# Optimization experiments

Measured on AMD Instinct MI355X. Metric: run time of the kernel, lower is better.

Reference implementation:

```python
import jax, jax.numpy as jnp
import numpy as np

N, B, S, BW, IC = 512, 4, 31, 11, 32

def gelu(x):
    return jax.nn.gelu(x, approximate=False)

def conv2d(x, w, b, pad, groups=1):
    y = jax.lax.conv_general_dilated(x, w, (1, 1), [(pad, pad), (pad, pad)],
        dimension_numbers=('NCHW', 'OIHW', 'NCHW'), feature_group_count=groups)
    return y + b[None, :, None, None]

def extract_windows(fmap, pos, win):
    C, H, W = fmap.shape[1:]
    r = win // 2
    cx = jnp.round(pos[:, 0]).astype(jnp.int32)
    cy = jnp.round(pos[:, 1]).astype(jnp.int32)
    off = jnp.arange(win, dtype=jnp.int32) - r
    ys = jnp.clip(cy[:, None] + off[None, :], 0, H - 1)
    xs = jnp.clip(cx[:, None] + off[None, :], 0, W - 1)
    w = fmap[0][:, ys[:, :, None], xs[:, None, :]]
    return jnp.transpose(w, (1, 0, 2, 3))

def _forward(bottleneck, vis_stem, spv, ppb,
             ic1_w, ic1_b, ic2_w, ic2_b, ic3_w, ic3_b,
             cnx_dw_w, cnx_dw_b, cnx_ln_w, cnx_ln_b,
             cnx_pw1_w, cnx_pw1_b, cnx_pw2_w, cnx_pw2_b, cnx_gamma,
             bnp_w, bnp_b, band_embed, film_w, film_b,
             dec1_w, dec1_b, dec2_w, dec2_b, dec3_w, dec3_b,
             tile_h, tile_w, fused_h, fused_w, vis_h, vis_w):
    n = spv.shape[0]
    # intrinsic path: per-source stem window -> 3 convs
    sw = extract_windows(vis_stem, spv, S)                 # [N,64,S,S]
    h = gelu(conv2d(sw, ic1_w, ic1_b, 1))
    h = gelu(conv2d(h, ic2_w, ic2_b, 1))
    intrinsic = conv2d(h, ic3_w, ic3_b, 1)                 # [N,IC,S,S]
    # bottleneck context path (vis px -> fused px: scale by vis_scale/fused_scale)
    scale = 0.1 / 0.4
    pbn = spv * scale
    pbn = jnp.stack([jnp.clip(pbn[:, 0], 0.0, fused_w - 1.0),
                     jnp.clip(pbn[:, 1], 0.0, fused_h - 1.0)], axis=-1)
    bwin = extract_windows(bottleneck, pbn, BW)            # [N,256,BW,BW]
    d = conv2d(bwin, cnx_dw_w, cnx_dw_b, 3, groups=bwin.shape[1])
    d = jnp.transpose(d, (0, 2, 3, 1))                     # NHWC
    mu = d.mean(-1, keepdims=True)
    var = ((d - mu) ** 2).mean(-1, keepdims=True)
    d = (d - mu) / jnp.sqrt(var + 1e-6) * cnx_ln_w + cnx_ln_b
    d = gelu(d @ cnx_pw1_w.T + cnx_pw1_b)
    d = (d @ cnx_pw2_w.T + cnx_pw2_b) * cnx_gamma
    bwin = bwin + jnp.transpose(d, (0, 3, 1, 2))
    bn_feat = gelu(conv2d(bwin, bnp_w, bnp_b, 0))          # [N,64,BW,BW]
    # fixed gaussian-weighted pooling (sigma=0.4 on [-1,1] grid)
    lin = jnp.linspace(-1.0, 1.0, BW)
    yy, xx = jnp.meshgrid(lin, lin, indexing='ij')
    g = jnp.exp(-(xx ** 2 + yy ** 2) / (2 * 0.4 ** 2))
    g = g / g.sum()
    bn_vec = (bn_feat * g[None, None]).sum((-2, -1))       # [N,64]
    # FiLM conditioning
    tile_pos = jnp.clip(jnp.stack([ppb[..., 0] / max(tile_w - 1.0, 1.0),
                                   ppb[..., 1] / max(tile_h - 1.0, 1.0)], -1), 0.0, 1.0)
    sub_px = ppb - jnp.round(ppb)
    band_e = jnp.broadcast_to(band_embed[None], (n, B, band_embed.shape[1]))
    bn_nb = jnp.broadcast_to(bn_vec[:, None], (n, B, bn_vec.shape[1]))
    cond = jnp.concatenate([band_e, tile_pos, sub_px, bn_nb], axis=-1)  # [N,B,84]
    film = cond @ film_w.T + film_b                        # [N,B,2*IC]
    gamma = 1.0 + film[..., :IC]
    beta = film[..., IC:]
    mod = intrinsic[:, None] * gamma[..., None, None] + beta[..., None, None]
    mod = gelu(mod).reshape(n * B, IC, S, S)
    o = gelu(conv2d(mod, dec1_w, dec1_b, 1))
    o = gelu(conv2d(o, dec2_w, dec2_b, 1))
    o = conv2d(o, dec3_w, dec3_b, 0).reshape(n, B, S, S)
    o = jax.nn.softplus(o)
    sums = jnp.maximum(o.sum((-2, -1), keepdims=True), 1e-8)
    return o / sums

def setup_inputs():
    key = jax.random.key(0)
    ks = jax.random.split(key, 24)
    FH = FW = 256; VH = VW = 1024; TH = TW = 1024
    f32 = jnp.float32
    nrm = lambda k, shp, s=0.05: jax.random.normal(k, shp, dtype=f32) * s
    return {
        'bottleneck': nrm(ks[0], (1, 256, FH, FW), 1.0),
        'vis_stem': nrm(ks[1], (1, 64, VH, VW), 1.0),
        'source_positions_vis': jax.random.uniform(ks[2], (N, 2), dtype=f32, minval=0.0, maxval=VW - 1.0),
        'positions_per_band': jax.random.uniform(ks[3], (N, B, 2), dtype=f32, minval=0.0, maxval=TW - 1.0),
        'ic1_w': nrm(ks[4], (64, 64, 3, 3)), 'ic1_b': jnp.zeros((64,), f32),
        'ic2_w': nrm(ks[5], (64, 64, 3, 3)), 'ic2_b': jnp.zeros((64,), f32),
        'ic3_w': nrm(ks[6], (IC, 64, 3, 3)), 'ic3_b': jnp.zeros((IC,), f32),
        'cnx_dw_w': nrm(ks[7], (256, 1, 7, 7)), 'cnx_dw_b': jnp.zeros((256,), f32),
        'cnx_ln_w': jnp.ones((256,), f32), 'cnx_ln_b': jnp.zeros((256,), f32),
        'cnx_pw1_w': nrm(ks[8], (1024, 256)), 'cnx_pw1_b': jnp.zeros((1024,), f32),
        'cnx_pw2_w': nrm(ks[9], (256, 1024)), 'cnx_pw2_b': jnp.zeros((256,), f32),
        'cnx_gamma': jnp.full((256,), 0.1, f32),
        'bnp_w': nrm(ks[10], (64, 256, 1, 1)), 'bnp_b': jnp.zeros((64,), f32),
        'band_embed': nrm(ks[11], (B, 16), 1.0),
        'film_w': nrm(ks[12], (2 * IC, 84)), 'film_b': jnp.zeros((2 * IC,), f32),
        'dec1_w': nrm(ks[13], (32, IC, 3, 3)), 'dec1_b': jnp.zeros((32,), f32),
        'dec2_w': nrm(ks[14], (32, 32, 3, 3)), 'dec2_b': jnp.zeros((32,), f32),
        'dec3_w': nrm(ks[15], (1, 32, 1, 1)), 'dec3_b': jnp.zeros((1,), f32),
        'tile_h': TH, 'tile_w': TW, 'fused_h': FH, 'fused_w': FW, 'vis_h': VH, 'vis_w': VW,
    }

def reference(bottleneck, vis_stem, source_positions_vis, positions_per_band, ic1_w, ic1_b, ic2_w, ic2_b, ic3_w, ic3_b, cnx_dw_w, cnx_dw_b, cnx_ln_w, cnx_ln_b, cnx_pw1_w, cnx_pw1_b, cnx_pw2_w, cnx_pw2_b, cnx_gamma, bnp_w, bnp_b, band_embed, film_w, film_b, dec1_w, dec1_b, dec2_w, dec2_b, dec3_w, dec3_b, tile_h, tile_w, fused_h, fused_w, vis_h, vis_w):
    return _forward(bottleneck, vis_stem, source_positions_vis, positions_per_band, ic1_w, ic1_b, ic2_w, ic2_b, ic3_w, ic3_b, cnx_dw_w, cnx_dw_b, cnx_ln_w, cnx_ln_b, cnx_pw1_w, cnx_pw1_b, cnx_pw2_w, cnx_pw2_b, cnx_gamma, bnp_w, bnp_b, band_embed, film_w, film_b, dec1_w, dec1_b, dec2_w, dec2_b, dec3_w, dec3_b, tile_h, tile_w, fused_h, fused_w, vis_h, vis_w)
```

## Files before the change

### kernel.cpp

```cpp
#include <hip/hip_runtime.h>
#include <cstdint>
#include <cstddef>
#include <cmath>

#define DEV __device__ __forceinline__

typedef __attribute__((ext_vector_type(8))) short bf16x8;
typedef __attribute__((ext_vector_type(4))) float f32x4;

DEV float erf_fast(float x){
  float ax = fabsf(x);
  float t = __builtin_amdgcn_rcpf(fmaf(0.3275911f, ax, 1.f));
  float p = t*fmaf(t, fmaf(t, fmaf(t, fmaf(t, 1.061405429f, -1.453152027f),
             1.421413741f), -0.284496736f), 0.254829592f);
  float e = __expf(-ax*ax);
  float r = fmaf(-p, e, 1.f);
  return x >= 0.f ? r : -r;
}
DEV float gelu_f(float x){ return 0.5f*x*(1.0f + erf_fast(x*0.7071067811865476f)); }
DEV float softplus_f(float x){ return fmaxf(x,0.f) + log1pf(expf(-fabsf(x))); }
DEV unsigned short f2bf(float x){
  unsigned u = __float_as_uint(x);
  unsigned r = (u + 0x7fffu + ((u>>16)&1u)) >> 16;
  return (unsigned short)r;
}
DEV float bf2f(unsigned short h){
  unsigned u = ((unsigned)h) << 16;
  return __uint_as_float(u);
}

struct PackJobs {
  const float* src[8];
  unsigned short* dst[8];
  int ntn[8], ntk[8], K[8], conv[8], base[8];
};

__global__ __launch_bounds__(256) void packall_k(PackJobs J)
{
  int blk = blockIdx.x;
  int j = 0;
#pragma unroll
  for (int i=1;i<8;++i) if (blk >= J.base[i]) j = i;
  int tid = (blk - J.base[j])*256 + threadIdx.x;
  const int ntk = J.ntk[j], K = J.K[j];
  int total = J.ntn[j]*ntk*64;
  if (tid >= total) return;
  int lane = tid & 63;
  int f = tid >> 6;
  int kt = f % ntk, nt = f / ntk;
  int row = nt*16 + (lane & 15);
  int k0 = kt*32 + (lane >> 4)*8;
  const float* src = J.src[j];
  unsigned short h[8];
  if (J.conv[j]) {
    const int Cin = K;
#pragma unroll
    for (int q=0;q<8;++q) {
      int k = k0 + q;
      int s = k / Cin;
      int ic = k - s*Cin;
      h[q] = f2bf(src[((size_t)row*Cin + ic)*9 + s]);
    }
  } else {
#pragma unroll
    for (int q=0;q<8;++q) h[q] = f2bf(src[(size_t)row*K + k0 + q]);
  }
  uint4 pk;
  pk.x = (unsigned)h[0] | ((unsigned)h[1]<<16);
  pk.y = (unsigned)h[2] | ((unsigned)h[3]<<16);
  pk.z = (unsigned)h[4] | ((unsigned)h[5]<<16);
  pk.w = (unsigned)h[6] | ((unsigned)h[7]<<16);
  *reinterpret_cast<uint4*>(J.dst[j] + (size_t)tid*8) = pk;
}

__global__ __launch_bounds__(256) void dwt_k(const float* __restrict__ w,
                                             float* __restrict__ wT)
{
  int k = blockIdx.x;
  int ch = threadIdx.x;
  wT[k*256 + ch] = w[(size_t)ch*49 + k];
}

__global__ __launch_bounds__(256) void extvwin_k(const float* __restrict__ vis,
                                                 const float* __restrict__ spv,
                                                 unsigned short* __restrict__ vwin)
{
  int il = blockIdx.x;
  int p = blockIdx.y*256 + threadIdx.x;
  if (p >= 1089) return;
  int wy = p/33, wx = p%33;
  unsigned short* dst = vwin + ((size_t)il*1089 + p)*64;
  if (wy==0 || wy==32 || wx==0 || wx==32) {
    uint4 z = {0,0,0,0};
#pragma unroll
    for (int q=0;q<8;++q) *reinterpret_cast<uint4*>(dst + q*8) = z;
    return;
  }
  int cx = (int)rintf(spv[il*2+0]);
  int cy = (int)rintf(spv[il*2+1]);
  int gy = min(max(cy + wy - 16, 0), 1023);
  int gx = min(max(cx + wx - 16, 0), 1023);
  const float* sp = vis + (size_t)gy*1024 + gx;
  unsigned short h[64];
#pragma unroll
  for (int c=0;c<64;++c) h[c] = f2bf(sp[(size_t)c<<20]);
#pragma unroll
  for (int q=0;q<8;++q) {
    uint4 pk;
    pk.x = (unsigned)h[q*8+0] | ((unsigned)h[q*8+1]<<16);
    pk.y = (unsigned)h[q*8+2] | ((unsigned)h[q*8+3]<<16);
    pk.z = (unsigned)h[q*8+4] | ((unsigned)h[q*8+5]<<16);
    pk.w = (unsigned)h[q*8+6] | ((unsigned)h[q*8+7]<<16);
    *reinterpret_cast<uint4*>(dst + q*8) = pk;
  }
}

template<int CIN, int COUT, int NKT, int MODE, bool FGELU>
__global__ __launch_bounds__(256,3) void convmf_k(
    const unsigned short* __restrict__ src,
    const unsigned short* __restrict__ Wp,
    const float* __restrict__ Bv,
    unsigned short* __restrict__ out)
{
  constexpr int NOCT = COUT/16;
  constexpr int NSLOT = CIN/8;
  constexpr int SWM = NSLOT-1;
  const int item = blockIdx.x;
  const int y0 = blockIdx.y*8;
  const int t = threadIdx.x;
  const int w = t>>6, l = t&63, g = l>>4, l15 = l&15;

  __shared__ __align__(16) unsigned short lds[330*CIN];

  for (int u = t; u < 330*NSLOT; u += 256) {
    int slot = u & SWM;
    int rowi = u / NSLOT;
    int r = rowi / 33, col = rowi - r*33;
    uint4 val = {0,0,0,0};
    if (MODE==1) {
      int gr = y0 + r;
      if (gr < 33)
        val = *reinterpret_cast<const uint4*>(src + ((size_t)item*1089 + gr*33 + col)*CIN + slot*8);
    } else {
      int y = y0 + r - 1, x = col - 1;
      if ((unsigned)y < 31u && (unsigned)x < 31u)
        val = *reinterpret_cast<const uint4*>(src + ((size_t)item*961 + y*31 + x)*CIN + slot*8);
    }
    int ds = slot ^ (rowi & SWM);
    *reinterpret_cast<uint4*>(&lds[rowi*CIN + ds*8]) = val;
  }
  __syncthreads();

  int pbase[4], gpos[4]; bool pvalid[4];
#pragma unroll
  for (int pt=0; pt<4; ++pt) {
    int p = (w*4+pt)*16 + l15;
    int pc = min(p, 247);
    int py = pc/31, px = pc - py*31;
    pbase[pt] = py*33 + px;
    gpos[pt] = y0*31 + p;
    pvalid[pt] = (p < 248) && (gpos[pt] < 961);
  }

  f32x4 acc[NOCT][4];
#pragma unroll
  for (int o=0;o<NOCT;++o)
#pragma unroll
    for (int pt=0;pt<4;++pt) acc[o][pt] = (f32x4){0.f,0.f,0.f,0.f};

  bf16x8 wcur[NOCT];
#pragma unroll
  for (int o=0;o<NOCT;++o)
    wcur[o] = *reinterpret_cast<const bf16x8*>(Wp + ((size_t)(o*NKT)*64 + l)*8);

  for (int kt=0; kt<NKT; ++kt) {
    bf16x8 wnxt[NOCT];
    if (kt+1 < NKT) {
#pragma unroll
      for (int o=0;o<NOCT;++o)
        wnxt[o] = *reinterpret_cast<const bf16x8*>(Wp + ((size_t)(o*NKT+kt+1)*64 + l)*8);
    }
    int k0 = kt*32 + g*8;
    int s = k0 / CIN;
    int icg = (k0 - s*CIN) >> 3;
    int roff = (s/3)*33 + (s - (s/3)*3);
    bf16x8 bf[4];
#pragma unroll
    for (int pt=0; pt<4; ++pt) {
      int rowi = pbase[pt] + roff;
      int ds = icg ^ (rowi & SWM);
      bf[pt] = *reinterpret_cast<const bf16x8*>(&lds[rowi*CIN + ds*8]);
    }
#pragma unroll
    for (int o=0; o<NOCT; ++o) {
#pragma unroll
      for (int pt=0; pt<4; ++pt)
        acc[o][pt] = __builtin_amdgcn_mfma_f32_16x16x32_bf16(wcur[o], bf[pt], acc[o][pt], 0,0,0);
    }
    if (kt+1 < NKT) {
#pragma unroll
      for (int o=0;o<NOCT;++o) wcur[o] = wnxt[o];
    }
  }

#pragma unroll
  for (int o=0; o<NOCT; ++o) {
    float4 bv4 = *reinterpret_cast<const float4*>(Bv + o*16 + g*4);
#pragma unroll
    for (int pt=0; pt<4; ++pt) {
      if (!pvalid[pt]) continue;
      float v0 = acc[o][pt][0] + bv4.x;
      float v1 = acc[o][pt][1] + bv4.y;
      float v2 = acc[o][pt][2] + bv4.z;
      float v3 = acc[o][pt][3] + bv4.w;
      if (FGELU) { v0=gelu_f(v0); v1=gelu_f(v1); v2=gelu_f(v2); v3=gelu_f(v3); }
      uint2 pk;
      pk.x = (unsigned)f2bf(v0) | ((unsigned)f2bf(v1)<<16);
      pk.y = (unsigned)f2bf(v2) | ((unsigned)f2bf(v3)<<16);
      *reinterpret_cast<uint2*>(out + ((size_t)item*961 + gpos[pt])*COUT + o*16 + g*4) = pk;
    }
  }
}

__global__ __launch_bounds__(256,3) void decfused_k(
    const unsigned short* __restrict__ intc,
    const unsigned short* __restrict__ Wp1, const float* __restrict__ B1,
    const unsigned short* __restrict__ Wp2, const float* __restrict__ B2,
    const float* __restrict__ film,
    const float* __restrict__ w3, const float* __restrict__ b3,
    float* __restrict__ outf, float* __restrict__ sums)
{
  const int item = blockIdx.x;
  const int y0 = blockIdx.y*8;
  const int t = threadIdx.x;
  const int w = t>>6, l = t&63, g = l>>4, l15 = l&15;

  __shared__ __align__(16) unsigned short ldsA[12*33*32];
  __shared__ __align__(16) unsigned short ldsB[10*33*32];

  const int sit = item >> 2;
  const float* frow = film + (size_t)item*64;

  for (int u=t; u<1320; u+=256)
    *reinterpret_cast<uint4*>(ldsB + u*8) = (uint4){0,0,0,0};

  for (int u=t; u<1584; u+=256) {
    int slot = u & 3;
    int rowi = u >> 2;
    int r = rowi/33, col = rowi - r*33;
    int y = y0 + r - 2, x = col - 1;
    uint4 val = {0,0,0,0};
    if ((unsigned)y < 31u && (unsigned)x < 31u) {
      val = *reinterpret_cast<const uint4*>(intc + ((size_t)sit*961 + y*31 + x)*32 + slot*8);
      int c0 = slot*8;
      float4 g0 = *reinterpret_cast<const float4*>(frow + c0);
      float4 g1 = *reinterpret_cast<const float4*>(frow + c0 + 4);
      float4 b0 = *reinterpret_cast<const float4*>(frow + 32 + c0);
      float4 b1 = *reinterpret_cast<const float4*>(frow + 32 + c0 + 4);
      unsigned short x8[8] = {
        (unsigned short)(val.x&0xffff),(unsigned short)(val.x>>16),
        (unsigned short)(val.y&0xffff),(unsigned short)(val.y>>16),
        (unsigned short)(val.z&0xffff),(unsigned short)(val.z>>16),
        (unsigned short)(val.w&0xffff),(unsigned short)(val.w>>16)};
      unsigned short o8[8];
      o8[0]=f2bf(gelu_f(fmaf(bf2f(x8[0]), 1.f+g0.x, b0.x)));
      o8[1]=f2bf(gelu_f(fmaf(bf2f(x8[1]), 1.f+g0.y, b0.y)));
      o8[2]=f2bf(gelu_f(fmaf(bf2f(x8[2]), 1.f+g0.z, b0.z)));
      o8[3]=f2bf(gelu_f(fmaf(bf2f(x8[3]), 1.f+g0.w, b0.w)));
      o8[4]=f2bf(gelu_f(fmaf(bf2f(x8[4]), 1.f+g1.x, b1.x)));
      o8[5]=f2bf(gelu_f(fmaf(bf2f(x8[5]), 1.f+g1.y, b1.y)));
      o8[6]=f2bf(gelu_f(fmaf(bf2f(x8[6]), 1.f+g1.z, b1.z)));
      o8[7]=f2bf(gelu_f(fmaf(bf2f(x8[7]), 1.f+g1.w, b1.w)));
      val.x = (unsigned)o8[0] | ((unsigned)o8[1]<<16);
      val.y = (unsigned)o8[2] | ((unsigned)o8[3]<<16);
      val.z = (unsigned)o8[4] | ((unsigned)o8[5]<<16);
      val.w = (unsigned)o8[6] | ((unsigned)o8[7]<<16);
    }
    int ds = slot ^ (rowi & 3);
    *reinterpret_cast<uint4*>(&ldsA[rowi*32 + ds*8]) = val;
  }
  __syncthreads();

  {
    int pbase[5], rowB[5]; bool pv[5];
#pragma unroll
    for (int pt=0; pt<5; ++pt) {
      int pd = (w*5+pt)*16 + l15;
      int pc = min(pd, 309);
      int ry = pc/31, rx = pc - ry*31;
      pbase[pt] = ry*33 + rx;
      rowB[pt] = ry*33 + rx + 1;
      int gy = y0 - 1 + ry;
      pv[pt] = (pd < 310) && ((unsigned)gy < 31u);
    }
    f32x4 a1[2][5];
#pragma unroll
    for (int o=0;o<2;++o)
#pragma unroll
      for (int pt=0;pt<5;++pt) a1[o][pt] = (f32x4){0.f,0.f,0.f,0.f};

    for (int kt=0; kt<9; ++kt) {
      int roff = (kt/3)*33 + (kt - (kt/3)*3);
      bf16x8 bf[5];
#pragma unroll
      for (int pt=0; pt<5; ++pt) {
        int rowi = pbase[pt] + roff;
        int ds = g ^ (rowi & 3);
        bf[pt] = *reinterpret_cast<const bf16x8*>(&ldsA[rowi*32 + ds*8]);
      }
#pragma unroll
      for (int o=0; o<2; ++o) {
        bf16x8 af = *reinterpret_cast<const bf16x8*>(Wp1 + ((size_t)(o*9+kt)*64 + l)*8);
#pragma unroll
        for (int pt=0; pt<5; ++pt)
          a1[o][pt] = __builtin_amdgcn_mfma_f32_16x16x32_bf16(af, bf[pt], a1[o][pt], 0,0,0);
      }
    }
#pragma unroll
    for (int o=0; o<2; ++o) {
      float4 bv4 = *reinterpret_cast<const float4*>(B1 + o*16 + g*4);
      int sl = o*2 + (g>>1);
#pragma unroll
      for (int pt=0; pt<5; ++pt) {
        if (!pv[pt]) continue;
        float v0 = gelu_f(a1[o][pt][0] + bv4.x);
        float v1 = gelu_f(a1[o][pt][1] + bv4.y);
        float v2 = gelu_f(a1[o][pt][2] + bv4.z);
        float v3 = gelu_f(a1[o][pt][3] + bv4.w);
        uint2 pk;
        pk.x = (unsigned)f2bf(v0) | ((unsigned)f2bf(v1)<<16);
        pk.y = (unsigned)f2bf(v2) | ((unsigned)f2bf(v3)<<16);
        int phys = sl ^ (rowB[pt] & 3);
        *reinterpret_cast<uint2*>(&ldsB[rowB[pt]*32 + phys*8 + (g&1)*4]) = pk;
      }
    }
  }
  __syncthreads();

  float bsum = 0.f;
  {
    int pbase[4], gpos[4]; bool pv[4];
#pragma unroll
    for (int pt=0; pt<4; ++pt) {
      int pd = (w*4+pt)*16 + l15;
      int pc = min(pd, 247);
      int py = pc/31, px = pc - py*31;
      pbase[pt] = py*33 + px;
      gpos[pt] = y0*31 + pd;
      pv[pt] = (pd < 248) && (gpos[pt] < 961);
    }
    f32x4 a2[2][4];
#pragma unroll
    for (int o=0;o<2;++o)
#pragma unroll
      for (int pt=0;pt<4;++pt) a2[o][pt] = (f32x4){0.f,0.f,0.f,0.f};

    for (int kt=0; kt<9; ++kt) {
      int roff = (kt/3)*33 + (kt - (kt/3)*3);
      bf16x8 bf[4];
#pragma unroll
      for (int pt=0; pt<4; ++pt) {
        int rowi = pbase[pt] + roff;
        int ds = g ^ (rowi & 3);
        bf[pt] = *reinterpret_cast<const bf16x8*>(&ldsB[rowi*32 + ds*8]);
      }
#pragma unroll
      for (int o=0; o<2; ++o) {
        bf16x8 af = *reinterpret_cast<const bf16x8*>(Wp2 + ((size_t)(o*9+kt)*64 + l)*8);
#pragma unroll
        for (int pt=0; pt<4; ++pt)
          a2[o][pt] = __builtin_amdgcn_mfma_f32_16x16x32_bf16(af, bf[pt], a2[o][pt], 0,0,0);
      }
    }

    float w3r[8];
#pragma unroll
    for (int o=0;o<2;++o) {
      float4 wv = *reinterpret_cast<const float4*>(w3 + o*16 + g*4);
      w3r[o*4+0]=wv.x; w3r[o*4+1]=wv.y; w3r[o*4+2]=wv.z; w3r[o*4+3]=wv.w;
    }
    float b3v = b3[0];
#pragma unroll
    for (int pt=0; pt<4; ++pt) {
      float part = 0.f;
#pragma unroll
      for (int o=0; o<2; ++o) {
        float4 bv4 = *reinterpret_cast<const float4*>(B2 + o*16 + g*4);
        float v0 = gelu_f(a2[o][pt][0] + bv4.x);
        float v1 = gelu_f(a2[o][pt][1] + bv4.y);
        float v2 = gelu_f(a2[o][pt][2] + bv4.z);
        float v3 = gelu_f(a2[o][pt][3] + bv4.w);
        part += v0*w3r[o*4+0] + v1*w3r[o*4+1] + v2*w3r[o*4+2] + v3*w3r[o*4+3];
      }
      part += __shfl_xor(part, 16);
      part += __shfl_xor(part, 32);
      float sp = softplus_f(part + b3v);
      if (pv[pt] && g==0) {
        outf[(size_t)item*961 + gpos[pt]] = sp;
        bsum += sp;
      }
    }
  }
  {
    float* redf = reinterpret_cast<float*>(ldsA);
    redf[t] = bsum;
    __syncthreads();
    for (int off=128; off>0; off>>=1) {
      if (t < off) redf[t] += redf[t+off];
      __syncthreads();
    }
    if (t==0) atomicAdd(&sums[item], redf[0]);
  }
}

__global__ __launch_bounds__(256,4) void dwfused4_k(
    const float* __restrict__ bott, const float* __restrict__ spv,
    const float* __restrict__ wT, const float* __restrict__ b,
    unsigned short* __restrict__ bwinT, unsigned short* __restrict__ dwout)
{
  const int n = blockIdx.x, cs = blockIdx.y*64, t = threadIdx.x;
  __shared__ float tile[121*66];

  float pxf = fminf(fmaxf(spv[n*2+0]*0.25f, 0.f), 255.f);
  float pyf = fminf(fmaxf(spv[n*2+1]*0.25f, 0.f), 255.f);
  int cx = (int)rintf(pxf), cy = (int)rintf(pyf);

  for (int idx=t; idx<121*32; idx+=256) {
    int j = idx/121, p = idx - j*121;
    int y = p/11, x = p - y*11;
    int gy = min(max(cy + y - 5, 0), 255);
    int gx = min(max(cx + x - 5, 0), 255);
    const float* s0 = bott + ((size_t)(cs+2*j)<<16) + (gy<<8) + gx;
    *reinterpret_cast<float2*>(&tile[p*66 + 2*j]) = (float2){s0[0], s0[65536]};
  }
  __syncthreads();

  for (int idx=t; idx<121*64; idx+=256) {
    int p = idx >> 6, c = idx & 63;
    bwinT[((size_t)n*121 + p)*256 + cs + c] = f2bf(tile[p*66 + c]);
  }

  const int c = t & 63, ph = t >> 6;
  const int ch = cs + c;
  const float bias = b[ch];

  for (int y=ph; y<11; y+=4) {
    float acc[11];
#pragma unroll
    for (int x=0;x<11;++x) acc[x] = bias;
#pragma unroll
    for (int dy=0; dy<7; ++dy) {
      int yy = y + dy - 3;
      if ((unsigned)yy < 11u) {
        float r[11];
#pragma unroll
        for (int k=0;k<11;++k) r[k] = tile[(yy*11+k)*66 + c];
        float w7[7];
#pragma unroll
        for (int j=0;j<7;++j) w7[j] = wT[(dy*7+j)*256 + ch];
#pragma unroll
        for (int x=0;x<11;++x) {
#pragma unroll
          for (int dx=0;dx<7;++dx) {
            int xx = x + dx - 3;
            if (xx >= 0 && xx < 11)
              acc[x] = fmaf(r[xx], w7[dx], acc[x]);
          }
        }
      }
    }
#pragma unroll
    for (int x=0;x<11;++x)
      dwout[((size_t)n*121 + y*11 + x)*256 + ch] = f2bf(acc[x]);
  }
}

__global__ __launch_bounds__(512,4) void cnx_mfma3_k(
    const unsigned short* __restrict__ xin,
    const float* __restrict__ lnw, const float* __restrict__ lnb,
    const unsigned short* __restrict__ W1p, const float* __restrict__ B1,
    const unsigned short* __restrict__ W2p, const float* __restrict__ B2,
    const float* __restrict__ gvec,
    const unsigned short* __restrict__ bwinT,
    const unsigned short* __restrict__ Wbp, const float* __restrict__ bnpb,
    float* __restrict__ bnv, float inv_gsum)
{
  const int t = threadIdx.x;
  const int w = t >> 6;
  const int l = t & 63;
  const int g = l >> 4;
  const int l15 = l & 15;
  const int row0 = blockIdx.x * 64;

  __shared__ __align__(16) unsigned short xs[64*264];
  __shared__ __align__(16) unsigned short hs[64*136];

  {
    const int rl = t >> 3, q = t & 7;
    const unsigned short* xr = xin + (size_t)(row0+rl)*256 + q*32;
    float xv[32]; float s = 0.f, s2 = 0.f;
#pragma unroll
    for (int i=0;i<32;i+=8){
      uint4 v = *reinterpret_cast<const uint4*>(xr+i);
      unsigned short xh[8] = {
        (unsigned short)(v.x&0xffff),(unsigned short)(v.x>>16),
        (unsigned short)(v.y&0xffff),(unsigned short)(v.y>>16),
        (unsigned short)(v.z&0xffff),(unsigned short)(v.z>>16),
        (unsigned short)(v.w&0xffff),(unsigned short)(v.w>>16)};
#pragma unroll
      for (int j=0;j<8;++j){
        float f = bf2f(xh[j]);
        xv[i+j] = f; s += f; s2 += f*f;
      }
    }
    s += __shfl_xor(s,1); s2 += __shfl_xor(s2,1);
    s += __shfl_xor(s,2); s2 += __shfl_xor(s2,2);
    s += __shfl_xor(s,4); s2 += __shfl_xor(s2,4);
    float mu = s*(1.f/256.f);
    float rstd = rsqrtf(s2*(1.f/256.f) - mu*mu + 1e-6f);
#pragma unroll
    for (int i=0;i<32;i+=8){
      int c = q*32 + i;
      float4 w0 = *reinterpret_cast<const float4*>(lnw+c);
      float4 w1 = *reinterpret_cast<const float4*>(lnw+c+4);
      float4 b0 = *reinterpret_cast<const float4*>(lnb+c);
      float4 b1 = *reinterpret_cast<const float4*>(lnb+c+4);
      unsigned short h[8];
      h[0]=f2bf(fmaf((xv[i+0]-mu)*rstd, w0.x, b0.x));
      h[1]=f2bf(fmaf((xv[i+1]-mu)*rstd, w0.y, b0.y));
      h[2]=f2bf(fmaf((xv[i+2]-mu)*rstd, w0.z, b0.z));
      h[3]=f2bf(fmaf((xv[i+3]-mu)*rstd, w0.w, b0.w));
      h[4]=f2bf(fmaf((xv[i+4]-mu)*rstd, w1.x, b1.x));
      h[5]=f2bf(fmaf((xv[i+5]-mu)*rstd, w1.y, b1.y));
      h[6]=f2bf(fmaf((xv[i+6]-mu)*rstd, w1.z, b1.z));
      h[7]=f2bf(fmaf((xv[i+7]-mu)*rstd, w1.w, b1.w));
      uint4 pk;
      pk.x = (unsigned)h[0] | ((unsigned)h[1]<<16);
      pk.y = (unsigned)h[2] | ((unsigned)h[3]<<16);
      pk.z = (unsigned)h[4] | ((unsigned)h[5]<<16);
      pk.w = (unsigned)h[6] | ((unsigned)h[7]<<16);
      *reinterpret_cast<uint4*>(&xs[rl*264 + c]) = pk;
    }
  }
  __syncthreads();

  f32x4 acc2[8];
#pragma unroll
  for (int i=0;i<8;++i) acc2[i] = (f32x4){0.f,0.f,0.f,0.f};

  for (int hc=0; hc<8; ++hc) {
    const int ht = hc*8 + w;
    f32x4 acc1[4];
#pragma unroll
    for (int i=0;i<4;++i) acc1[i] = (f32x4){0.f,0.f,0.f,0.f};

#pragma unroll
    for (int kt=0; kt<8; ++kt) {
      bf16x8 xf[4];
#pragma unroll
      for (int rt=0; rt<4; ++rt)
        xf[rt] = *reinterpret_cast<const bf16x8*>(&xs[(rt*16+l15)*264 + kt*32 + g*8]);
      bf16x8 wf = *reinterpret_cast<const bf16x8*>(W1p + ((size_t)(ht*8+kt)*64 + l)*8);
#pragma unroll
      for (int rt=0; rt<4; ++rt)
        acc1[rt] = __builtin_amdgcn_mfma_f32_16x16x32_bf16(wf, xf[rt], acc1[rt], 0,0,0);
    }
    {
      const int hb = hc*128 + w*16 + 4*g;
      float4 b1v = *reinterpret_cast<const float4*>(B1 + hb);
#pragma unroll
      for (int rt=0; rt<4; ++rt) {
        unsigned short h0 = f2bf(gelu_f(acc1[rt][0] + b1v.x));
        unsigned short h1 = f2bf(gelu_f(acc1[rt][1] + b1v.y));
        unsigned short h2 = f2bf(gelu_f(acc1[rt][2] + b1v.z));
        unsigned short h3 = f2bf(gelu_f(acc1[rt][3] + b1v.w));
        uint2 pk;
        pk.x = (unsigned)h0 | ((unsigned)h1<<16);
        pk.y = (unsigned)h2 | ((unsigned)h3<<16);
        *reinterpret_cast<uint2*>(&hs[(rt*16+l15)*136 + w*16 + 4*g]) = pk;
      }
    }
    __syncthreads();
#pragma unroll
    for (int kt=0; kt<4; ++kt) {
      bf16x8 hf[4];
#pragma unroll
      for (int rt=0; rt<4; ++rt)
        hf[rt] = *reinterpret_cast<const bf16x8*>(&hs[(rt*16+l15)*136 + kt*32 + g*8]);
#pragma unroll
      for (int cj=0; cj<2; ++cj) {
        const int ct = 2*w + cj;
        bf16x8 wf = *reinterpret_cast<const bf16x8*>(W2p + ((size_t)(ct*32 + hc*4 + kt)*64 + l)*8);
#pragma unroll
        for (int rt=0; rt<4; ++rt)
          acc2[cj*4+rt] = __builtin_amdgcn_mfma_f32_16x16x32_bf16(hf[rt], wf, acc2[cj*4+rt], 0,0,0);
      }
    }
    __syncthreads();
  }

#pragma unroll
  for (int cj=0; cj<2; ++cj) {
    const int c = (2*w+cj)*16 + l15;
    const float b2 = B2[c], gm = gvec[c];
#pragma unroll
    for (int rt=0; rt<4; ++rt) {
#pragma unroll
      for (int reg=0; reg<4; ++reg) {
        int row = rt*16 + 4*g + reg;
        float res = bf2f(bwinT[(size_t)(row0+row)*256 + c]) + (acc2[cj*4+rt][reg] + b2)*gm;
        xs[row*264 + c] = f2bf(res);
      }
    }
  }
  __syncthreads();

  {
    const int oct = w & 3;
    f32x4 abn[2];
#pragma unroll
    for (int i=0;i<2;++i) abn[i] = (f32x4){0.f,0.f,0.f,0.f};
#pragma unroll
    for (int kt=0; kt<8; ++kt) {
      bf16x8 bfw = *reinterpret_cast<const bf16x8*>(Wbp + ((size_t)(oct*8+kt)*64 + l)*8);
#pragma unroll
      for (int i=0;i<2;++i) {
        const int rt = (w>>2) + 2*i;
        bf16x8 af = *reinterpret_cast<const bf16x8*>(&xs[(rt*16+l15)*264 + kt*32 + g*8]);
        abn[i] = __builtin_amdgcn_mfma_f32_16x16x32_bf16(af, bfw, abn[i], 0,0,0);
      }
    }

    float* red = reinterpret_cast<float*>(hs);
#pragma unroll
    for (int i=0;i<2;++i) {
      const int rt = (w>>2) + 2*i;
      float bv = bnpb[oct*16 + l15];
#pragma unroll
      for (int reg=0; reg<4; ++reg) {
        int lr = rt*16 + g*4 + reg;
        int p = (row0 + lr) % 121;
        int py=p/11, px=p-py*11;
        float ly=-1.f+0.2f*py, lx=-1.f+0.2f*px;
        float wg = __expf(-(lx*lx+ly*ly)/0.32f) * inv_gsum;
        red[lr*64 + oct*16 + l15] = gelu_f(abn[i][reg] + bv) * wg;
      }
    }
  }
  __syncthreads();
  {
    float* red = reinterpret_cast<float*>(hs);
    int oc = t & 63, seg = t >> 6;
    float s = 0.f;
    int curn = (row0 + seg*8) / 121;
    for (int i=0;i<8;++i) {
      int row = seg*8 + i;
      int n = (row0 + row) / 121;
      if (n != curn) { atomicAdd(&bnv[curn*64 + oc], s); s = 0.f; curn = n; }
      s += red[row*64 + oc];
    }
    atomicAdd(&bnv[curn*64 + oc], s);
  }
}

__global__ __launch_bounds__(256) void film_k(
    const float* __restrict__ bn_vec, const float* __restrict__ ppb,
    const float* __restrict__ bemb, const float* __restrict__ fw,
    const float* __restrict__ fb, float* __restrict__ film)
{
  int n = blockIdx.x, t = threadIdx.x;
  __shared__ float cond[4][84];
  for (int i=t; i<4*84; i+=256) {
    int b = i/84, j = i%84;
    float v;
    if (j < 16) v = bemb[b*16 + j];
    else if (j == 16) { float p = ppb[((size_t)n*4+b)*2+0]; v = fminf(fmaxf(p*(1.f/1023.f),0.f),1.f); }
    else if (j == 17) { float p = ppb[((size_t)n*4+b)*2+1]; v = fminf(fmaxf(p*(1.f/1023.f),0.f),1.f); }
    else if (j == 18) { float p = ppb[((size_t)n*4+b)*2+0]; v = p - rintf(p); }
    else if (j == 19) { float p = ppb[((size_t)n*4+b)*2+1]; v = p - rintf(p); }
    else v = bn_vec[n*64 + (j-20)];
    cond[b][j] = v;
  }
  __syncthreads();
  int b = t >> 6, oc = t & 63;
  float s = fb[oc];
  for (int j=0;j<84;++j) s = fmaf(cond[b][j], fw[oc*84+j], s);
  film[((size_t)n*4+b)*64 + oc] = s;
}

__global__ __launch_bounds__(256) void norm_k(float* __restrict__ out,
                                              const float* __restrict__ sums)
{
  int il = blockIdx.x;
  int p = blockIdx.y*256 + threadIdx.x;
  if (p < 961) {
    float inv = 1.f / fmaxf(sums[il], 1e-8f);
    out[(size_t)il*961 + p] *= inv;
  }
}

extern "C" void kernel_launch(void* const* d_in, const int* in_sizes, int n_in,
                              void* d_out, int out_size, void* d_ws, size_t ws_size,
                              hipStream_t stream)
{
  const float* bott = (const float*)d_in[0];
  const float* vis  = (const float*)d_in[1];
  const float* spv  = (const float*)d_in[2];
  const float* ppb  = (const float*)d_in[3];
  const float* ic1w = (const float*)d_in[4];  const float* ic1b = (const float*)d_in[5];
  const float* ic2w = (const float*)d_in[6];  const float* ic2b = (const float*)d_in[7];
  const float* ic3w = (const float*)d_in[8];  const float* ic3b = (const float*)d_in[9];
  const float* dww  = (const float*)d_in[10]; const float* dwb  = (const float*)d_in[11];
  const float* lnw  = (const float*)d_in[12]; const float* lnb  = (const float*)d_in[13];
  const float* pw1w = (const float*)d_in[14]; const float* pw1b = (const float*)d_in[15];
  const float* pw2w = (const float*)d_in[16]; const float* pw2b = (const float*)d_in[17];
  const float* cgam = (const float*)d_in[18];
  const float* bnpw = (const float*)d_in[19]; const float* bnpb = (const float*)d_in[20];
  const float* bemb = (const float*)d_in[21];
  const float* fw   = (const float*)d_in[22]; const float* fb   = (const float*)d_in[23];
  const float* d1w  = (const float*)d_in[24]; const float* d1b  = (const float*)d_in[25];
  const float* d2w  = (const float*)d_in[26]; const float* d2b  = (const float*)d_in[27];
  const float* d3w  = (const float*)d_in[28]; const float* d3b  = (const float*)d_in[29];
  float* out = (float*)d_out;

  char* ws = (char*)d_ws;

  const int CH = (ws_size >= 116500000ull) ? 256 : 128;

  unsigned short* bwinT = (unsigned short*)(ws);
  unsigned short* dwout = (unsigned short*)(ws + 31719424);
  unsigned short* vwin = (unsigned short*)(ws);
  size_t o_bufA = (size_t)CH*139392;
  size_t o_bufB = o_bufA + (size_t)CH*123008;
  size_t o_bufI = o_bufB + (size_t)CH*123008;
  size_t p1end  = o_bufI + (size_t)CH*61504;
  unsigned short* bufA = (unsigned short*)(ws + o_bufA);
  unsigned short* bufB = (unsigned short*)(ws + o_bufB);
  unsigned short* bufI = (unsigned short*)(ws + o_bufI);
  size_t tail = (p1end > 63438848ull) ? p1end : 63438848ull;

  float* bnv  = (float*)(ws + tail);
  float* sums = (float*)(ws + tail + 131072);
  float* film = (float*)(ws + tail + 139264);
  unsigned short* W1p = (unsigned short*)(ws + tail + 663552);
  unsigned short* W2p = (unsigned short*)(ws + tail + 1187840);
  unsigned short* Wbp = (unsigned short*)(ws + tail + 1712128);
  unsigned short* Pc1 = (unsigned short*)(ws + tail + 1744896);
  unsigned short* Pc2 = (unsigned short*)(ws + tail + 1818624);
  unsigned short* Pc3 = (unsigned short*)(ws + tail + 1892352);
  unsigned short* Pd1 = (unsigned short*)(ws + tail + 1929216);
  unsigned short* Pd2 = (unsigned short*)(ws + tail + 1947648);
  float* dwwT = (float*)(ws + tail + 1966080);

  {
    PackJobs J;
    const float* srcs[8] = {pw1w, pw2w, bnpw, ic1w, ic2w, ic3w, d1w, d2w};
    unsigned short* dsts[8] = {W1p, W2p, Wbp, Pc1, Pc2, Pc3, Pd1, Pd2};
    int ntns[8] = {64,16,4, 4,4,2, 2,2};
    int ntks[8] = {8,32,8, 18,18,18, 9,9};
    int Ks[8]   = {256,1024,256, 64,64,64, 32,32};
    int convs[8]= {0,0,0, 1,1,1, 1,1};
    int base = 0;
    for (int i=0;i<8;++i) {
      J.src[i]=srcs[i]; J.dst[i]=dsts[i]; J.ntn[i]=ntns[i]; J.ntk[i]=ntks[i];
      J.K[i]=Ks[i]; J.conv[i]=convs[i]; J.base[i]=base;
      base += (ntns[i]*ntks[i]*64 + 255)/256;
    }
    packall_k<<<base,256,0,stream>>>(J);
  }
  dwt_k<<<49,256,0,stream>>>(dww, dwwT);

  hipMemsetAsync(ws + tail, 0, 139264, stream);

  float gs = 0.f;
  for (int py=0; py<11; ++py) for (int px=0; px<11; ++px) {
    float ly=-1.f+0.2f*py, lx=-1.f+0.2f*px;
    gs += expf(-(lx*lx+ly*ly)/0.32f);
  }
  const float inv_gsum = 1.f/gs;

  dwfused4_k<<<dim3(512,4),256,0,stream>>>(bott, spv, dwwT, dwb, bwinT, dwout);
  cnx_mfma3_k<<<968,512,0,stream>>>(dwout, lnw,lnb, W1p,pw1b, W2p,pw2b, cgam,
                                    bwinT, Wbp, bnpb, bnv, inv_gsum);
  film_k<<<512,256,0,stream>>>(bnv, ppb, bemb, fw, fb, film);

  for (int n0 = 0; n0 < 512; n0 += CH) {
    extvwin_k<<<dim3(CH,5),256,0,stream>>>(vis, spv + n0*2, vwin);
    convmf_k<64,64,18,1,true ><<<dim3(CH,4),256,0,stream>>>(vwin, Pc1, ic1b, bufA);
    convmf_k<64,64,18,0,true ><<<dim3(CH,4),256,0,stream>>>(bufA, Pc2, ic2b, bufB);
    convmf_k<64,32,18,0,false><<<dim3(CH,4),256,0,stream>>>(bufB, Pc3, ic3b, bufI);
    decfused_k<<<dim3(CH*4,4),256,0,stream>>>(bufI, Pd1, d1b, Pd2, d2b,
        film + (size_t)n0*4*64, d3w, d3b,
        out + (size_t)n0*4*961, sums + n0*4);
  }
  norm_k<<<dim3(2048,4),256,0,stream>>>(out, sums);
}
```

Baseline: 774.2 us.

## Fuse three intrinsic convs into one LDS-resident kernel with halo recompute

```diff
diff --git a/kernel.cpp b/kernel.cpp
--- a/kernel.cpp
+++ b/kernel.cpp
@@ -115,109 +115,214 @@
   }
 }
 
-template<int CIN, int COUT, int NKT, int MODE, bool FGELU>
-__global__ __launch_bounds__(256,3) void convmf_k(
-    const unsigned short* __restrict__ src,
-    const unsigned short* __restrict__ Wp,
-    const float* __restrict__ Bv,
-    unsigned short* __restrict__ out)
-{
-  constexpr int NOCT = COUT/16;
-  constexpr int NSLOT = CIN/8;
-  constexpr int SWM = NSLOT-1;
+__global__ __launch_bounds__(512,2) void convchain_k(
+    const unsigned short* __restrict__ vwin,
+    const unsigned short* __restrict__ Wp1, const float* __restrict__ B1,
+    const unsigned short* __restrict__ Wp2, const float* __restrict__ B2,
+    const unsigned short* __restrict__ Wp3, const float* __restrict__ B3,
+    unsigned short* __restrict__ outI)
+{
   const int item = blockIdx.x;
   const int y0 = blockIdx.y*8;
   const int t = threadIdx.x;
   const int w = t>>6, l = t&63, g = l>>4, l15 = l&15;
 
-  __shared__ __align__(16) unsigned short lds[330*CIN];
-
-  for (int u = t; u < 330*NSLOT; u += 256) {
-    int slot = u & SWM;
-    int rowi = u / NSLOT;
-    int r = rowi / 33, col = rowi - r*33;
-    uint4 val = {0,0,0,0};
-    if (MODE==1) {
-      int gr = y0 + r;
-      if (gr < 33)
-        val = *reinterpret_cast<const uint4*>(src + ((size_t)item*1089 + gr*33 + col)*CIN + slot*8);
-    } else {
-      int y = y0 + r - 1, x = col - 1;
-      if ((unsigned)y < 31u && (unsigned)x < 31u)
-        val = *reinterpret_cast<const uint4*>(src + ((size_t)item*961 + y*31 + x)*CIN + slot*8);
-    }
-    int ds = slot ^ (rowi & SWM);
-    *reinterpret_cast<uint4*>(&lds[rowi*CIN + ds*8]) = val;
-  }
-  __syncthreads();
-
-  int pbase[4], gpos[4]; bool pvalid[4];
-#pragma unroll
-  for (int pt=0; pt<4; ++pt) {
-    int p = (w*4+pt)*16 + l15;
-    int pc = min(p, 247);
-    int py = pc/31, px = pc - py*31;
-    pbase[pt] = py*33 + px;
-    gpos[pt] = y0*31 + p;
-    pvalid[pt] = (p < 248) && (gpos[pt] < 961);
-  }
-
-  f32x4 acc[NOCT][4];
-#pragma unroll
-  for (int o=0;o<NOCT;++o)
-#pragma unroll
-    for (int pt=0;pt<4;++pt) acc[o][pt] = (f32x4){0.f,0.f,0.f,0.f};
-
-  bf16x8 wcur[NOCT];
-#pragma unroll
-  for (int o=0;o<NOCT;++o)
-    wcur[o] = *reinterpret_cast<const bf16x8*>(Wp + ((size_t)(o*NKT)*64 + l)*8);
-
-  for (int kt=0; kt<NKT; ++kt) {
-    bf16x8 wnxt[NOCT];
-    if (kt+1 < NKT) {
-#pragma unroll
-      for (int o=0;o<NOCT;++o)
-        wnxt[o] = *reinterpret_cast<const bf16x8*>(Wp + ((size_t)(o*NKT+kt+1)*64 + l)*8);
-    }
-    int k0 = kt*32 + g*8;
-    int s = k0 / CIN;
-    int icg = (k0 - s*CIN) >> 3;
-    int roff = (s/3)*33 + (s - (s/3)*3);
-    bf16x8 bf[4];
-#pragma unroll
-    for (int pt=0; pt<4; ++pt) {
-      int rowi = pbase[pt] + roff;
-      int ds = icg ^ (rowi & SWM);
-      bf[pt] = *reinterpret_cast<const bf16x8*>(&lds[rowi*CIN + ds*8]);
-    }
-#pragma unroll
-    for (int o=0; o<NOCT; ++o) {
-#pragma unroll
-      for (int pt=0; pt<4; ++pt)
-        acc[o][pt] = __builtin_amdgcn_mfma_f32_16x16x32_bf16(wcur[o], bf[pt], acc[o][pt], 0,0,0);
-    }
-    if (kt+1 < NKT) {
-#pragma unroll
-      for (int o=0;o<NOCT;++o) wcur[o] = wnxt[o];
-    }
-  }
-
-#pragma unroll
-  for (int o=0; o<NOCT; ++o) {
-    float4 bv4 = *reinterpret_cast<const float4*>(Bv + o*16 + g*4);
-#pragma unroll
-    for (int pt=0; pt<4; ++pt) {
-      if (!pvalid[pt]) continue;
-      float v0 = acc[o][pt][0] + bv4.x;
-      float v1 = acc[o][pt][1] + bv4.y;
-      float v2 = acc[o][pt][2] + bv4.z;
-      float v3 = acc[o][pt][3] + bv4.w;
-      if (FGELU) { v0=gelu_f(v0); v1=gelu_f(v1); v2=gelu_f(v2); v3=gelu_f(v3); }
-      uint2 pk;
-      pk.x = (unsigned)f2bf(v0) | ((unsigned)f2bf(v1)<<16);
-      pk.y = (unsigned)f2bf(v2) | ((unsigned)f2bf(v3)<<16);
-      *reinterpret_cast<uint2*>(out + ((size_t)item*961 + gpos[pt])*COUT + o*16 + g*4) = pk;
+  __shared__ __align__(16) unsigned short bufIn[462*64];
+  __shared__ __align__(16) unsigned short bufC1[396*64];
+  unsigned short* bufC2 = bufIn;
+
+  const uint4 z4 = {0,0,0,0};
+
+  for (int u=t; u<396*8; u+=512)
+    *reinterpret_cast<uint4*>(bufC1 + u*8) = z4;
+  for (int u=t; u<462*8; u+=512) {
+    int slot = u & 7;
+    int rowi = u >> 3;
+    int r = rowi/33;
+    int wy = y0 - 2 + r;
+    uint4 val = z4;
+    if ((unsigned)wy < 33u)
+      val = *reinterpret_cast<const uint4*>(
+          vwin + ((size_t)item*1089 + wy*33 + (rowi - r*33))*64 + slot*8);
+    int ds = slot ^ (rowi & 7);
+    *reinterpret_cast<uint4*>(&bufIn[rowi*64 + ds*8]) = val;
+  }
+  __syncthreads();
+
+  {
+    int pbase[3], rowB[3]; bool pv[3];
+#pragma unroll
+    for (int pt=0; pt<3; ++pt) {
+      int pd = (w*3+pt)*16 + l15;
+      int pc = min(pd, 371);
+      int ry = pc/31, rx = pc - ry*31;
+      pbase[pt] = ry*33 + rx;
+      rowB[pt] = ry*33 + rx + 1;
+      int yab = y0 - 2 + ry;
+      pv[pt] = (pd < 372) && ((unsigned)yab < 31u);
+    }
+    f32x4 a1[4][3];
+#pragma unroll
+    for (int o=0;o<4;++o)
+#pragma unroll
+      for (int pt=0;pt<3;++pt) a1[o][pt] = (f32x4){0.f,0.f,0.f,0.f};
+
+    for (int kt=0; kt<18; ++kt) {
+      int k0 = kt*32 + g*8;
+      int s = k0 >> 6;
+      int icg = (k0 - (s<<6)) >> 3;
+      int roff = (s/3)*33 + (s - (s/3)*3);
+      bf16x8 bf[3];
+#pragma unroll
+      for (int pt=0; pt<3; ++pt) {
+        int rowi = pbase[pt] + roff;
+        int ds = icg ^ (rowi & 7);
+        bf[pt] = *reinterpret_cast<const bf16x8*>(&bufIn[rowi*64 + ds*8]);
+      }
+#pragma unroll
+      for (int o=0; o<4; ++o) {
+        bf16x8 af = *reinterpret_cast<const bf16x8*>(Wp1 + ((size_t)(o*18+kt)*64 + l)*8);
+#pragma unroll
+        for (int pt=0; pt<3; ++pt)
+          a1[o][pt] = __builtin_amdgcn_mfma_f32_16x16x32_bf16(af, bf[pt], a1[o][pt], 0,0,0);
+      }
+    }
+#pragma unroll
+    for (int o=0; o<4; ++o) {
+      float4 bv4 = *reinterpret_cast<const float4*>(B1 + o*16 + g*4);
+      int sl = o*2 + (g>>1);
+#pragma unroll
+      for (int pt=0; pt<3; ++pt) {
+        if (!pv[pt]) continue;
+        float v0 = gelu_f(a1[o][pt][0] + bv4.x);
+        float v1 = gelu_f(a1[o][pt][1] + bv4.y);
+        float v2 = gelu_f(a1[o][pt][2] + bv4.z);
+        float v3 = gelu_f(a1[o][pt][3] + bv4.w);
+        uint2 pk;
+        pk.x = (unsigned)f2bf(v0) | ((unsigned)f2bf(v1)<<16);
+        pk.y = (unsigned)f2bf(v2) | ((unsigned)f2bf(v3)<<16);
+        int phys = sl ^ (rowB[pt] & 7);
+        *reinterpret_cast<uint2*>(&bufC1[rowB[pt]*64 + phys*8 + (g&1)*4]) = pk;
+      }
+    }
+  }
+  __syncthreads();
+
+  for (int u=t; u<330*8; u+=512)
+    *reinterpret_cast<uint4*>(bufC2 + u*8) = z4;
+  __syncthreads();
+
+  {
+    int pbase[3], rowB[3]; bool pv[3];
+#pragma unroll
+    for (int pt=0; pt<3; ++pt) {
+      int pd = (w*3+pt)*16 + l15;
+      int pc = min(pd, 309);
+      int ry = pc/31, rx = pc - ry*31;
+      pbase[pt] = ry*33 + rx;
+      rowB[pt] = ry*33 + rx + 1;
+      int yab = y0 - 1 + ry;
+      pv[pt] = (pd < 310) && ((unsigned)yab < 31u);
+    }
+    f32x4 a2[4][3];
+#pragma unroll
+    for (int o=0;o<4;++o)
+#pragma unroll
+      for (int pt=0;pt<3;++pt) a2[o][pt] = (f32x4){0.f,0.f,0.f,0.f};
+
+    for (int kt=0; kt<18; ++kt) {
+      int k0 = kt*32 + g*8;
+      int s = k0 >> 6;
+      int icg = (k0 - (s<<6)) >> 3;
+      int roff = (s/3)*33 + (s - (s/3)*3);
+      bf16x8 bf[3];
+#pragma unroll
+      for (int pt=0; pt<3; ++pt) {
+        int rowi = pbase[pt] + roff;
+        int ds = icg ^ (rowi & 7);
+        bf[pt] = *reinterpret_cast<const bf16x8*>(&bufC1[rowi*64 + ds*8]);
+      }
+#pragma unroll
+      for (int o=0; o<4; ++o) {
+        bf16x8 af = *reinterpret_cast<const bf16x8*>(Wp2 + ((size_t)(o*18+kt)*64 + l)*8);
+#pragma unroll
+        for (int pt=0; pt<3; ++pt)
+          a2[o][pt] = __builtin_amdgcn_mfma_f32_16x16x32_bf16(af, bf[pt], a2[o][pt], 0,0,0);
+      }
+    }
+#pragma unroll
+    for (int o=0; o<4; ++o) {
+      float4 bv4 = *reinterpret_cast<const float4*>(B2 + o*16 + g*4);
+      int sl = o*2 + (g>>1);
+#pragma unroll
+      for (int pt=0; pt<3; ++pt) {
+        if (!pv[pt]) continue;
+        float v0 = gelu_f(a2[o][pt][0] + bv4.x);
+        float v1 = gelu_f(a2[o][pt][1] + bv4.y);
+        float v2 = gelu_f(a2[o][pt][2] + bv4.z);
+        float v3 = gelu_f(a2[o][pt][3] + bv4.w);
+        uint2 pk;
+        pk.x = (unsigned)f2bf(v0) | ((unsigned)f2bf(v1)<<16);
+        pk.y = (unsigned)f2bf(v2) | ((unsigned)f2bf(v3)<<16);
+        int phys = sl ^ (rowB[pt] & 7);
+        *reinterpret_cast<uint2*>(&bufC2[rowB[pt]*64 + phys*8 + (g&1)*4]) = pk;
+      }
+    }
+  }
+  __syncthreads();
+
+  {
+    int pbase[2], gpos[2]; bool pv[2];
+#pragma unroll
+    for (int pt=0; pt<2; ++pt) {
+      int pd = (w*2+pt)*16 + l15;
+      int pc = min(pd, 247);
+      int ry = pc/31, rx = pc - ry*31;
+      pbase[pt] = ry*33 + rx;
+      gpos[pt] = y0*31 + pd;
+      pv[pt] = (pd < 248) && (gpos[pt] < 961);
+    }
+    f32x4 a3[2][2];
+#pragma unroll
+    for (int o=0;o<2;++o)
+#pragma unroll
+      for (int pt=0;pt<2;++pt) a3[o][pt] = (f32x4){0.f,0.f,0.f,0.f};
+
+    for (int kt=0; kt<18; ++kt) {
+      int k0 = kt*32 + g*8;
+      int s = k0 >> 6;
+      int icg = (k0 - (s<<6)) >> 3;
+      int roff = (s/3)*33 + (s - (s/3)*3);
+      bf16x8 bf[2];
+#pragma unroll
+      for (int pt=0; pt<2; ++pt) {
+        int rowi = pbase[pt] + roff;
+        int ds = icg ^ (rowi & 7);
+        bf[pt] = *reinterpret_cast<const bf16x8*>(&bufC2[rowi*64 + ds*8]);
+      }
+#pragma unroll
+      for (int o=0; o<2; ++o) {
+        bf16x8 af = *reinterpret_cast<const bf16x8*>(Wp3 + ((size_t)(o*18+kt)*64 + l)*8);
+#pragma unroll
+        for (int pt=0; pt<2; ++pt)
+          a3[o][pt] = __builtin_amdgcn_mfma_f32_16x16x32_bf16(af, bf[pt], a3[o][pt], 0,0,0);
+      }
+    }
+#pragma unroll
+    for (int o=0; o<2; ++o) {
+      float4 bv4 = *reinterpret_cast<const float4*>(B3 + o*16 + g*4);
+#pragma unroll
+      for (int pt=0; pt<2; ++pt) {
+        if (!pv[pt]) continue;
+        float v0 = a3[o][pt][0] + bv4.x;
+        float v1 = a3[o][pt][1] + bv4.y;
+        float v2 = a3[o][pt][2] + bv4.z;
+        float v3 = a3[o][pt][3] + bv4.w;
+        uint2 pk;
+        pk.x = (unsigned)f2bf(v0) | ((unsigned)f2bf(v1)<<16);
+        pk.y = (unsigned)f2bf(v2) | ((unsigned)f2bf(v3)<<16);
+        *reinterpret_cast<uint2*>(outI + ((size_t)item*961 + gpos[pt])*32 + o*16 + g*4) = pk;
+      }
     }
   }
 }
@@ -725,19 +830,11 @@
 
   char* ws = (char*)d_ws;
 
-  const int CH = (ws_size >= 116500000ull) ? 256 : 128;
-
   unsigned short* bwinT = (unsigned short*)(ws);
   unsigned short* dwout = (unsigned short*)(ws + 31719424);
-  unsigned short* vwin = (unsigned short*)(ws);
-  size_t o_bufA = (size_t)CH*139392;
-  size_t o_bufB = o_bufA + (size_t)CH*123008;
-  size_t o_bufI = o_bufB + (size_t)CH*123008;
-  size_t p1end  = o_bufI + (size_t)CH*61504;
-  unsigned short* bufA = (unsigned short*)(ws + o_bufA);
-  unsigned short* bufB = (unsigned short*)(ws + o_bufB);
-  unsigned short* bufI = (unsigned short*)(ws + o_bufI);
-  size_t tail = (p1end > 63438848ull) ? p1end : 63438848ull;
+  unsigned short* vwin  = (unsigned short*)(ws);
+  unsigned short* bufI  = (unsigned short*)(ws + 71368704);
+  size_t tail = 102858752;
 
   float* bnv  = (float*)(ws + tail);
   float* sums = (float*)(ws + tail + 131072);
@@ -784,14 +881,9 @@
                                     bwinT, Wbp, bnpb, bnv, inv_gsum);
   film_k<<<512,256,0,stream>>>(bnv, ppb, bemb, fw, fb, film);
 
-  for (int n0 = 0; n0 < 512; n0 += CH) {
-    extvwin_k<<<dim3(CH,5),256,0,stream>>>(vis, spv + n0*2, vwin);
-    convmf_k<64,64,18,1,true ><<<dim3(CH,4),256,0,stream>>>(vwin, Pc1, ic1b, bufA);
-    convmf_k<64,64,18,0,true ><<<dim3(CH,4),256,0,stream>>>(bufA, Pc2, ic2b, bufB);
-    convmf_k<64,32,18,0,false><<<dim3(CH,4),256,0,stream>>>(bufB, Pc3, ic3b, bufI);
-    decfused_k<<<dim3(CH*4,4),256,0,stream>>>(bufI, Pd1, d1b, Pd2, d2b,
-        film + (size_t)n0*4*64, d3w, d3b,
-        out + (size_t)n0*4*961, sums + n0*4);
-  }
+  extvwin_k<<<dim3(512,5),256,0,stream>>>(vis, spv, vwin);
+  convchain_k<<<dim3(512,4),512,0,stream>>>(vwin, Pc1,ic1b, Pc2,ic2b, Pc3,ic3b, bufI);
+  decfused_k<<<dim3(2048,4),256,0,stream>>>(bufI, Pd1,d1b, Pd2,d2b,
+      film, d3w, d3b, out, sums);
   norm_k<<<dim3(2048,4),256,0,stream>>>(out, sums);
 }
```

After: 752.2 us. -2.9%, faster.
